# Optimization experiments

Measured on AMD Instinct MI355X. Metric: run time of the kernel, lower is better.

Reference implementation:

```python
import jax, jax.numpy as jnp
import numpy as np

N = 100000        # nodes
E = 1600000       # directed edges (before self loops)
F = 128           # input node features
H1, H2, H3 = 64, 32, 16
G = 64            # graphs in batch
EPS = 1e-5
NEG_SLOPE = 0.2


def setup_inputs():
    key = jax.random.key(0)
    ks = jax.random.split(key, 16)
    def rn(k, shape, scale=1.0):
        return jax.random.normal(k, shape, dtype=jnp.float32) * scale
    inp = {}
    inp['x'] = rn(ks[0], (N, F))
    inp['edge_index'] = jax.random.randint(ks[1], (2, E), 0, N)
    inp['batch'] = jnp.sort(jax.random.randint(ks[2], (N,), 0, G))
    dims = [(F, H1), (H1, H2), (H2, H3)]
    i = 3
    for li, (fi, fo) in enumerate(dims, start=1):
        s = 1.0 / np.sqrt(fi)
        kk = jax.random.split(ks[i], 3)
        inp[f'Wl{li}'] = rn(kk[0], (fi, fo), s)
        inp[f'bl{li}'] = jnp.zeros((fo,), jnp.float32)
        inp[f'Wr{li}'] = rn(kk[1], (fi, fo), s)
        inp[f'br{li}'] = jnp.zeros((fo,), jnp.float32)
        inp[f'att{li}'] = rn(kk[2], (fo,), 1.0 / np.sqrt(fo))
        inp[f'bias{li}'] = jnp.zeros((fo,), jnp.float32)
        inp[f'gamma{li}'] = jnp.ones((fo,), jnp.float32)
        inp[f'beta{li}'] = jnp.zeros((fo,), jnp.float32)
        i += 1
    inp['linW'] = rn(ks[i], (H3, 1), 0.25)
    inp['linb'] = jnp.zeros((1,), jnp.float32)
    return inp


def _gatv2(x, Wl, bl, Wr, br, att, bias, src, dst):
    # PyG GATv2Conv, heads=1: e_ij = a^T LeakyReLU(Wl x_j + Wr x_i)
    xl = x @ Wl + bl                         # [N, H] source transform
    xr = x @ Wr + br                         # [N, H] target transform
    e = jax.nn.leaky_relu(xl[src] + xr[dst], NEG_SLOPE) @ att   # [E']
    # numerically stable segment softmax over incoming edges of dst
    emax = jax.ops.segment_max(e, dst, num_segments=N)
    w = jnp.exp(e - emax[dst])
    denom = jax.ops.segment_sum(w, dst, num_segments=N)
    alpha = w / (denom[dst] + 1e-16)         # [E']
    out = jax.ops.segment_sum(alpha[:, None] * xl[src], dst, num_segments=N)
    return out + bias


def _batchnorm(x, gamma, beta):
    mu = jnp.mean(x, axis=0)
    var = jnp.var(x, axis=0)
    return (x - mu) * jax.lax.rsqrt(var + EPS) * gamma + beta


def reference(x, edge_index, batch,
              Wl1, bl1, Wr1, br1, att1, bias1, gamma1, beta1,
              Wl2, bl2, Wr2, br2, att2, bias2, gamma2, beta2,
              Wl3, bl3, Wr3, br3, att3, bias3, gamma3, beta3,
              linW, linb):
    # add self loops once (PyG GATv2Conv default add_self_loops=True)
    loops = jnp.arange(N, dtype=edge_index.dtype)
    src = jnp.concatenate([edge_index[0], loops])
    dst = jnp.concatenate([edge_index[1], loops])

    h = _gatv2(x, Wl1, bl1, Wr1, br1, att1, bias1, src, dst)
    h = jax.nn.relu(_batchnorm(h, gamma1, beta1))
    h = _gatv2(h, Wl2, bl2, Wr2, br2, att2, bias2, src, dst)
    h = jax.nn.relu(_batchnorm(h, gamma2, beta2))
    h = _gatv2(h, Wl3, bl3, Wr3, br3, att3, bias3, src, dst)
    h = jax.nn.relu(_batchnorm(h, gamma3, beta3))

    # global mean pool over graphs
    sums = jax.ops.segment_sum(h, batch, num_segments=G)          # [G, 16]
    cnts = jax.ops.segment_sum(jnp.ones((N,), h.dtype), batch, num_segments=G)
    pooled = sums / jnp.maximum(cnts, 1.0)[:, None]
    return pooled @ linW + linb                                   # [G, 1]
```

## Files before the change

kernel.cpp:

```cpp
#include <hip/hip_runtime.h>
#include <hip/hip_bf16.h>


static constexpr int G_ = 64;

typedef short bfrag __attribute__((ext_vector_type(8)));
typedef float facc  __attribute__((ext_vector_type(4)));

__device__ __forceinline__ float asfloat_(unsigned int u) {
  union { unsigned int i; float f; } c; c.i = u; return c.f;
}
__device__ __forceinline__ unsigned short f2bf(float f) {
  union { float f; unsigned int i; } c;
  c.f = f;
  unsigned int r = c.i + 0x7FFFu + ((c.i >> 16) & 1u);
  return (unsigned short)(r >> 16);
}

__device__ __forceinline__ void load_bf4(const unsigned short* p, float* f) {
  uint2 q = *reinterpret_cast<const uint2*>(p);
  f[0] = asfloat_(q.x << 16); f[1] = asfloat_(q.x & 0xFFFF0000u);
  f[2] = asfloat_(q.y << 16); f[3] = asfloat_(q.y & 0xFFFF0000u);
}

__global__ __launch_bounds__(256) void pack_all(
    const float* __restrict__ Wl1, const float* __restrict__ Wr1,
    const float* __restrict__ bl1, const float* __restrict__ br1,
    const float* __restrict__ Wl2, const float* __restrict__ Wr2,
    const float* __restrict__ bl2, const float* __restrict__ br2,
    const float* __restrict__ Wl3, const float* __restrict__ Wr3,
    const float* __restrict__ bl3, const float* __restrict__ br3,
    unsigned short* __restrict__ Wt1, float* __restrict__ bc1,
    unsigned short* __restrict__ Wt2, float* __restrict__ bc2,
    unsigned short* __restrict__ Wt3, float* __restrict__ bc3) {
  int i = blockIdx.x * 256 + threadIdx.x;
  if (i < 128 * 128) { int c = i >> 7, k = i & 127;
    Wt1[i] = f2bf((c < 64) ? Wl1[k * 64 + c] : Wr1[k * 64 + (c - 64)]); }
  if (i < 128) bc1[i] = (i < 64) ? bl1[i] : br1[i - 64];
  if (i < 64 * 64) { int c = i >> 6, k = i & 63;
    Wt2[i] = f2bf((c < 32) ? Wl2[k * 32 + c] : Wr2[k * 32 + (c - 32)]); }
  if (i < 64) bc2[i] = (i < 32) ? bl2[i] : br2[i - 32];
  if (i < 32 * 32) { int c = i >> 5, k = i & 31;
    Wt3[i] = f2bf((c < 16) ? Wl3[k * 16 + c] : Wr3[k * 16 + (c - 16)]); }
  if (i < 32) bc3[i] = (i < 16) ? bl3[i] : br3[i - 16];
}

__global__ __launch_bounds__(256) void edge_hist(
    const int* __restrict__ ei, int* __restrict__ deg, int E, int Etot, int N) {
  int p = blockIdx.x & 7;
  int q = blockIdx.x >> 3;
  int nbq = gridDim.x >> 3;
  float scale = 8.0f / (float)N;
  for (int i = q * 256 + threadIdx.x; i < Etot; i += nbq * 256) {
    int dst = (i < E) ? ei[E + i] : (i - E);
    int pp = min((int)((float)dst * scale), 7);
    if (pp == p) atomicAdd(&deg[dst], 1);
  }
}

__global__ __launch_bounds__(256) void scan1(
    const int* __restrict__ deg, int* __restrict__ part, int* __restrict__ bsums, int n) {
  __shared__ int ts[256];
  int t = threadIdx.x, b = blockIdx.x;
  int base = b * 1024 + t * 4;
  int d[4];
#pragma unroll
  for (int q = 0; q < 4; q++) d[q] = (base + q < n) ? deg[base + q] : 0;
  int s = d[0] + d[1] + d[2] + d[3];
  ts[t] = s;
  __syncthreads();
  for (int o = 1; o < 256; o <<= 1) {
    int v = (t >= o) ? ts[t - o] : 0;
    __syncthreads();
    ts[t] += v;
    __syncthreads();
  }
  int incl = ts[t];
  if (t == 255) bsums[b] = incl;
  int run = incl - s;
#pragma unroll
  for (int q = 0; q < 4; q++) {
    if (base + q < n) part[base + q] = run;
    run += d[q];
  }
}

__global__ void scan2(int* bsums, int nb) {
  __shared__ int s[256];
  int t = threadIdx.x;
  int v = (t < nb) ? bsums[t] : 0;
  s[t] = v;
  __syncthreads();
  for (int o = 1; o < 256; o <<= 1) {
    int u = (t >= o) ? s[t - o] : 0;
    __syncthreads();
    s[t] += u;
    __syncthreads();
  }
  if (t < nb) bsums[t] = s[t] - v;
}

__global__ __launch_bounds__(256) void scan3(
    int* __restrict__ rp, int* __restrict__ cur, const int* __restrict__ bsums,
    int n, int Etot) {
  int i = blockIdx.x * 256 + threadIdx.x;
  if (i < n) {
    int v = rp[i] + bsums[i >> 10];
    rp[i] = v; cur[i] = v;
  }
  if (i == 0) rp[n] = Etot;
}

__global__ __launch_bounds__(256) void scatter_edges(
    const int* __restrict__ ei, int* __restrict__ cur, int* __restrict__ ssrc,
    int E, int Etot, int N) {
  int p = blockIdx.x & 7;
  int q = blockIdx.x >> 3;
  int nbq = gridDim.x >> 3;
  float scale = 8.0f / (float)N;
  for (int i = q * 256 + threadIdx.x; i < Etot; i += nbq * 256) {
    int dst = (i < E) ? ei[E + i] : (i - E);
    int pp = min((int)((float)dst * scale), 7);
    if (pp != p) continue;
    int src = (i < E) ? ei[i] : (i - E);
    int pos = atomicAdd(&cur[dst], 1);
    ssrc[pos] = src;
  }
}

template <int FI, int FO, int AMODE>
__global__ __launch_bounds__(256) void gemm_mfma(
    const void* __restrict__ Ain, const float* __restrict__ ssb,
    const unsigned short* __restrict__ Wt, const float* __restrict__ bcat,
    unsigned short* __restrict__ XL, unsigned short* __restrict__ XR, int N) {
  constexpr int NT = FO / 16;
  constexpr int KS = FI / 32;
  constexpr int H = FO / 2;
  int tid = threadIdx.x;
  int w = tid >> 6;
  int lr = tid & 15;
  int lg = (tid & 63) >> 4;
  int n0 = blockIdx.x * 64;
  int arow = min(n0 + w * 16 + lr, N - 1);

  facc acc[NT];
#pragma unroll
  for (int t = 0; t < NT; t++)
#pragma unroll
    for (int e = 0; e < 4; e++) acc[t][e] = 0.f;

#pragma unroll
  for (int ks = 0; ks < KS; ks++) {
    int k0 = ks * 32 + lg * 8;
    bfrag a;
    if constexpr (AMODE == 0) {
      const unsigned short* Ab = (const unsigned short*)Ain;
      a = *reinterpret_cast<const bfrag*>(&Ab[(size_t)arow * FI + k0]);
    } else {
      const float* Af = (const float*)Ain;
      const float* p = &Af[(size_t)arow * FI + k0];
      float4 lo = *reinterpret_cast<const float4*>(p);
      float4 hi = *reinterpret_cast<const float4*>(p + 4);
      float f[8] = {lo.x, lo.y, lo.z, lo.w, hi.x, hi.y, hi.z, hi.w};
      if constexpr (AMODE == 2) {
        float4 sc0 = *reinterpret_cast<const float4*>(&ssb[k0]);
        float4 sc1 = *reinterpret_cast<const float4*>(&ssb[k0 + 4]);
        float4 sh0 = *reinterpret_cast<const float4*>(&ssb[FI + k0]);
        float4 sh1 = *reinterpret_cast<const float4*>(&ssb[FI + k0 + 4]);
        float sc[8] = {sc0.x, sc0.y, sc0.z, sc0.w, sc1.x, sc1.y, sc1.z, sc1.w};
        float sh[8] = {sh0.x, sh0.y, sh0.z, sh0.w, sh1.x, sh1.y, sh1.z, sh1.w};
#pragma unroll
        for (int e = 0; e < 8; e++) f[e] = fmaxf(fmaf(f[e], sc[e], sh[e]), 0.f);
      }
      union { bfrag v; unsigned short u[8]; } cv;
#pragma unroll
      for (int e = 0; e < 8; e++) cv.u[e] = f2bf(f[e]);
      a = cv.v;
    }
#pragma unroll
    for (int t = 0; t < NT; t++) {
      bfrag b = *reinterpret_cast<const bfrag*>(&Wt[(size_t)(t * 16 + lr) * FI + k0]);
      acc[t] = __builtin_amdgcn_mfma_f32_16x16x32_bf16(a, b, acc[t], 0, 0, 0);
    }
  }

#pragma unroll
  for (int t = 0; t < NT; t++) {
    int col = t * 16 + lr;
    float bias = bcat[col];
    unsigned short* dstbuf = (t < NT / 2) ? XL : XR;
    int cc = (t < NT / 2) ? col : (col - H);
#pragma unroll
    for (int r = 0; r < 4; r++) {
      int n = n0 + w * 16 + lg * 4 + r;
      if (n < N) dstbuf[(size_t)n * H + cc] = f2bf(acc[t][r] + bias);
    }
  }
}

__device__ __forceinline__ float lrelu02(float z) {
  return fmaxf(z, 0.2f * z);
}

template <int H>
__global__ __launch_bounds__(256) void gat_agg5(
    const unsigned short* __restrict__ XL, const unsigned short* __restrict__ XR,
    const float* __restrict__ att, const float* __restrict__ bias,
    const int* __restrict__ rp, const int* __restrict__ ssrc,
    float* __restrict__ out, int N) {
  constexpr int L = H / 4;
  constexpr int C = 64 / L;
  constexpr int CHUNK = 128;
  __shared__ float ts[4][CHUNK];
  int wv = threadIdx.x >> 6;
  int v = blockIdx.x * 4 + wv;
  if (v >= N) return;
  int lane = threadIdx.x & 63;
  int fl = lane % L;
  int sub = lane / L;

  float xr[4];
  load_bf4(&XR[(size_t)v * H + fl * 4], xr);
  const float4 a4 = *reinterpret_cast<const float4*>(&att[fl * 4]);
  int beg = rp[v], end = rp[v + 1];

  float m = -3.0e38f, d = 0.f, acc[4] = {0.f, 0.f, 0.f, 0.f};

  for (int c0 = beg; c0 < end; c0 += CHUNK) {
    int n = min(CHUNK, end - c0);

    float mc = -3.0e38f;
    for (int k = sub; k < n; k += C) {
      int u = ssrc[c0 + k];
      float xl[4];
      load_bf4(&XL[(size_t)u * H + fl * 4], xl);
      float t = a4.x * lrelu02(xl[0] + xr[0]);
      t = fmaf(a4.y, lrelu02(xl[1] + xr[1]), t);
      t = fmaf(a4.z, lrelu02(xl[2] + xr[2]), t);
      t = fmaf(a4.w, lrelu02(xl[3] + xr[3]), t);
#pragma unroll
      for (int o = L / 2; o >= 1; o >>= 1) t += __shfl_xor(t, o);
      mc = fmaxf(mc, t);
      if (fl == 0) ts[wv][k] = t;
    }
#pragma unroll
    for (int o = L; o < 64; o <<= 1) mc = fmaxf(mc, __shfl_xor(mc, o));

    float mn = fmaxf(m, mc);
    float sc = __expf(m - mn);
    d *= sc;
#pragma unroll
    for (int e = 0; e < 4; e++) acc[e] *= sc;
    m = mn;

    float dl = 0.f;
    for (int k = lane; k < n; k += 64) {
      float w = __expf(ts[wv][k] - m);
      ts[wv][k] = w;
      dl += w;
    }
#pragma unroll
    for (int o = 1; o < 64; o <<= 1) dl += __shfl_xor(dl, o);
    d += dl;

    for (int k = sub; k < n; k += C) {
      float wgt = ts[wv][k];
      int u = ssrc[c0 + k];
      float xl[4];
      load_bf4(&XL[(size_t)u * H + fl * 4], xl);
#pragma unroll
      for (int e = 0; e < 4; e++) acc[e] = fmaf(wgt, xl[e], acc[e]);
    }
  }

#pragma unroll
  for (int o = L; o < 64; o <<= 1) {
#pragma unroll
    for (int e = 0; e < 4; e++) acc[e] += __shfl_xor(acc[e], o);
  }

  if (lane < L) {
    float inv = 1.f / (d + 1e-16f);
    const float4 b4 = *reinterpret_cast<const float4*>(&bias[fl * 4]);
    float4 o4 = make_float4(fmaf(acc[0], inv, b4.x), fmaf(acc[1], inv, b4.y),
                            fmaf(acc[2], inv, b4.z), fmaf(acc[3], inv, b4.w));
    *reinterpret_cast<float4*>(&out[(size_t)v * H + fl * 4]) = o4;
  }
}

template <int H>
__global__ __launch_bounds__(256) void bn_stats(
    const float* __restrict__ X, float* __restrict__ stats, int N) {
  __shared__ float ls[256], ls2[256];
  int tid = threadIdx.x;
  int h = tid % H;
  constexpr int RPB = 256 / H;
  int r0 = blockIdx.x * RPB + tid / H;
  float s = 0.f, s2 = 0.f;
  for (int n = r0; n < N; n += gridDim.x * RPB) {
    float val = X[(size_t)n * H + h];
    s += val; s2 += val * val;
  }
  ls[tid] = s; ls2[tid] = s2;
  __syncthreads();
  if (tid < H) {
    for (int g = 1; g < RPB; g++) { s += ls[tid + g * H]; s2 += ls2[tid + g * H]; }
    atomicAdd(&stats[h], s);
    atomicAdd(&stats[H + h], s2);
  }
}

__global__ void bn_finalize(
    const float* __restrict__ stats, const float* __restrict__ gamma,
    const float* __restrict__ beta, float* __restrict__ ss, int H, int N) {
  int h = threadIdx.x;
  if (h < H) {
    float mean = stats[h] / (float)N;
    float var = stats[H + h] / (float)N - mean * mean;
    float istd = rsqrtf(var + 1e-5f);
    float sc = gamma[h] * istd;
    ss[h] = sc;
    ss[H + h] = beta[h] - mean * sc;
  }
}

__global__ __launch_bounds__(256) void pool_kernel(
    const float* __restrict__ X, const float* __restrict__ ss,
    const int* __restrict__ batch, float* __restrict__ pool,
    float* __restrict__ cnt, int N) {
  __shared__ float lp[G_ * 16];
  __shared__ float lc[G_];
  int tid = threadIdx.x;
  for (int j = tid; j < G_ * 16; j += 256) lp[j] = 0.f;
  if (tid < G_) lc[tid] = 0.f;
  __syncthreads();
  int tot = N * 16;
  for (int i = blockIdx.x * 256 + tid; i < tot; i += gridDim.x * 256) {
    int n = i >> 4, h = i & 15;
    int g = batch[n];
    float t = X[i] * ss[h] + ss[16 + h];
    t = (t > 0.f) ? t : 0.f;
    atomicAdd(&lp[g * 16 + h], t);
    if (h == 0) atomicAdd(&lc[g], 1.0f);
  }
  __syncthreads();
  for (int j = tid; j < G_ * 16; j += 256) atomicAdd(&pool[j], lp[j]);
  if (tid < G_) atomicAdd(&cnt[tid], lc[tid]);
}

__global__ void final_linear(
    const float* __restrict__ pool, const float* __restrict__ cnt,
    const float* __restrict__ linW, const float* __restrict__ linb,
    float* __restrict__ out) {
  int g = threadIdx.x;
  if (g < G_) {
    float c = fmaxf(cnt[g], 1.0f);
    float acc = 0.f;
    for (int h = 0; h < 16; h++) acc += (pool[g * 16 + h] / c) * linW[h];
    out[g] = acc + linb[0];
  }
}

extern "C" void kernel_launch(void* const* d_in, const int* in_sizes, int n_in,
                              void* d_out, int out_size, void* d_ws, size_t ws_size,
                              hipStream_t stream) {
  const float* x = (const float*)d_in[0];
  const int* ei = (const int*)d_in[1];
  const int* batch = (const int*)d_in[2];
  const int N = in_sizes[0] / 128;
  const int E = in_sizes[1] / 2;
  const int Etot = E + N;

  char* wsb = (char*)d_ws;
  size_t off = 0;
  auto alloc = [&](size_t bytes) -> void* {
    void* p = wsb + off;
    off += (bytes + 255) & ~(size_t)255;
    return p;
  };
  unsigned short* XLb = (unsigned short*)alloc((size_t)64 * N * 2);
  unsigned short* XRb = (unsigned short*)alloc((size_t)64 * N * 2);
  float* R2 = (float*)alloc((size_t)64 * N * 4);
  int* row_ptr = (int*)alloc((size_t)(N + 1) * 4);
  int* cursor = (int*)alloc((size_t)N * 4);
  int* bsums = (int*)alloc(4096);
  int* ssrc = (int*)alloc((size_t)Etot * 4);
  unsigned short* Wt1 = (unsigned short*)alloc(16384 * 2);
  float* bc1 = (float*)alloc(128 * 4);
  unsigned short* Wt2 = (unsigned short*)alloc(4096 * 2);
  float* bc2 = (float*)alloc(64 * 4);
  unsigned short* Wt3 = (unsigned short*)alloc(1024 * 2);
  float* bc3 = (float*)alloc(32 * 4);
  float* ss = (float*)alloc(256 * 4);
  size_t zelems = (size_t)N + 3 * 128 + G_ * 16 + G_;
  char* zb = (char*)alloc(zelems * 4);
  int* deg = (int*)zb;
  float* stats1 = (float*)(zb + (size_t)N * 4);
  float* stats2 = stats1 + 128;
  float* stats3 = stats2 + 128;
  float* pool = stats3 + 128;
  float* cnt = pool + G_ * 16;

  const float* Wl1 = (const float*)d_in[3];  const float* bl1 = (const float*)d_in[4];
  const float* Wr1 = (const float*)d_in[5];  const float* br1 = (const float*)d_in[6];
  const float* att1 = (const float*)d_in[7]; const float* bias1 = (const float*)d_in[8];
  const float* g1 = (const float*)d_in[9];   const float* b1 = (const float*)d_in[10];
  const float* Wl2 = (const float*)d_in[11]; const float* bl2 = (const float*)d_in[12];
  const float* Wr2 = (const float*)d_in[13]; const float* br2 = (const float*)d_in[14];
  const float* att2 = (const float*)d_in[15]; const float* bias2 = (const float*)d_in[16];
  const float* g2 = (const float*)d_in[17];  const float* b2 = (const float*)d_in[18];
  const float* Wl3 = (const float*)d_in[19]; const float* bl3 = (const float*)d_in[20];
  const float* Wr3 = (const float*)d_in[21]; const float* br3 = (const float*)d_in[22];
  const float* att3 = (const float*)d_in[23]; const float* bias3 = (const float*)d_in[24];
  const float* g3 = (const float*)d_in[25];  const float* b3 = (const float*)d_in[26];
  const float* linW = (const float*)d_in[27]; const float* linb = (const float*)d_in[28];
  float* out = (float*)d_out;

  int nb = (N + 1023) / 1024;
  int nnodeblk = (N + 3) / 4;
  int ngemm = (N + 63) / 64;

  pack_all<<<64, 256, 0, stream>>>(Wl1, Wr1, bl1, br1, Wl2, Wr2, bl2, br2,
                                   Wl3, Wr3, bl3, br3, Wt1, bc1, Wt2, bc2, Wt3, bc3);
  hipMemsetAsync(zb, 0, zelems * 4, stream);

  edge_hist<<<4096, 256, 0, stream>>>(ei, deg, E, Etot, N);
  scan1<<<nb, 256, 0, stream>>>(deg, row_ptr, bsums, N);
  scan2<<<1, 256, 0, stream>>>(bsums, nb);
  scan3<<<(N + 255) / 256, 256, 0, stream>>>(row_ptr, cursor, bsums, N, Etot);
  scatter_edges<<<4096, 256, 0, stream>>>(ei, cursor, ssrc, E, Etot, N);

  gemm_mfma<128, 128, 1><<<ngemm, 256, 0, stream>>>(x, nullptr, Wt1, bc1, XLb, XRb, N);
  gat_agg5<64><<<nnodeblk, 256, 0, stream>>>(XLb, XRb, att1, bias1, row_ptr, ssrc, R2, N);
  bn_stats<64><<<512, 256, 0, stream>>>(R2, stats1, N);
  bn_finalize<<<1, 64, 0, stream>>>(stats1, g1, b1, ss, 64, N);

  gemm_mfma<64, 64, 2><<<ngemm, 256, 0, stream>>>(R2, ss, Wt2, bc2, XLb, XRb, N);
  gat_agg5<32><<<nnodeblk, 256, 0, stream>>>(XLb, XRb, att2, bias2, row_ptr, ssrc, R2, N);
  bn_stats<32><<<512, 256, 0, stream>>>(R2, stats2, N);
  bn_finalize<<<1, 64, 0, stream>>>(stats2, g2, b2, ss, 32, N);

  gemm_mfma<32, 32, 2><<<ngemm, 256, 0, stream>>>(R2, ss, Wt3, bc3, XLb, XRb, N);
  gat_agg5<16><<<nnodeblk, 256, 0, stream>>>(XLb, XRb, att3, bias3, row_ptr, ssrc, R2, N);
  bn_stats<16><<<512, 256, 0, stream>>>(R2, stats3, N);
  bn_finalize<<<1, 64, 0, stream>>>(stats3, g3, b3, ss, 16, N);

  pool_kernel<<<2048, 256, 0, stream>>>(R2, ss, batch, pool, cnt, N);
  final_linear<<<1, 64, 0, stream>>>(pool, cnt, linW, linb, out);
}
```

Measured before the change: 578.3 us.

## Keep gathered neighbor features in registers and fuse softmax passes in GAT aggregation

The aggregation kernel now loads each chunk of neighbor features once into registers (ITER edges per lane group). It computes scores, the online max, the exp weights and the weighted accumulation from those registers. This drops the shared-memory score buffer and the second gather of XL per edge. The denominator is kept per lane group and reduced with shuffles at the end. The costs are more registers per thread and wasted lanes when a node's degree is not a multiple of the chunk size; per-layer ITER values are chosen to balance these.

After: 502.4 us. 13.1% less time.

```diff
diff --git a/kernel.cpp b/kernel.cpp
--- a/kernel.cpp
+++ b/kernel.cpp
@@ -202,18 +202,16 @@
   return fmaxf(z, 0.2f * z);
 }
 
-template <int H>
-__global__ __launch_bounds__(256) void gat_agg5(
+template <int H, int ITER>
+__global__ __launch_bounds__(256) void gat_agg6(
     const unsigned short* __restrict__ XL, const unsigned short* __restrict__ XR,
     const float* __restrict__ att, const float* __restrict__ bias,
     const int* __restrict__ rp, const int* __restrict__ ssrc,
     float* __restrict__ out, int N) {
   constexpr int L = H / 4;
   constexpr int C = 64 / L;
-  constexpr int CHUNK = 128;
-  __shared__ float ts[4][CHUNK];
-  int wv = threadIdx.x >> 6;
-  int v = blockIdx.x * 4 + wv;
+  constexpr int CHUNK = C * ITER;
+  int v = blockIdx.x * 4 + (threadIdx.x >> 6);
   if (v >= N) return;
   int lane = threadIdx.x & 63;
   int fl = lane % L;
@@ -226,22 +224,25 @@
 
   float m = -3.0e38f, d = 0.f, acc[4] = {0.f, 0.f, 0.f, 0.f};
 
-  for (int c0 = beg; c0 < end; c0 += CHUNK) {
-    int n = min(CHUNK, end - c0);
-
+  for (int cb = beg; cb < end; cb += CHUNK) {
+    float xb[ITER][4];
+    float tl[ITER];
     float mc = -3.0e38f;
-    for (int k = sub; k < n; k += C) {
-      int u = ssrc[c0 + k];
-      float xl[4];
-      load_bf4(&XL[(size_t)u * H + fl * 4], xl);
-      float t = a4.x * lrelu02(xl[0] + xr[0]);
-      t = fmaf(a4.y, lrelu02(xl[1] + xr[1]), t);
-      t = fmaf(a4.z, lrelu02(xl[2] + xr[2]), t);
-      t = fmaf(a4.w, lrelu02(xl[3] + xr[3]), t);
+#pragma unroll
+    for (int it = 0; it < ITER; it++) {
+      int j = cb + it * C + sub;
+      bool valid = (j < end);
+      int jj = valid ? j : (end - 1);
+      int u = ssrc[jj];
+      load_bf4(&XL[(size_t)u * H + fl * 4], xb[it]);
+      float t = a4.x * lrelu02(xb[it][0] + xr[0]);
+      t = fmaf(a4.y, lrelu02(xb[it][1] + xr[1]), t);
+      t = fmaf(a4.z, lrelu02(xb[it][2] + xr[2]), t);
+      t = fmaf(a4.w, lrelu02(xb[it][3] + xr[3]), t);
 #pragma unroll
       for (int o = L / 2; o >= 1; o >>= 1) t += __shfl_xor(t, o);
-      mc = fmaxf(mc, t);
-      if (fl == 0) ts[wv][k] = t;
+      tl[it] = valid ? t : -3.0e38f;
+      mc = fmaxf(mc, tl[it]);
     }
 #pragma unroll
     for (int o = L; o < 64; o <<= 1) mc = fmaxf(mc, __shfl_xor(mc, o));
@@ -253,28 +254,18 @@
     for (int e = 0; e < 4; e++) acc[e] *= sc;
     m = mn;
 
-    float dl = 0.f;
-    for (int k = lane; k < n; k += 64) {
-      float w = __expf(ts[wv][k] - m);
-      ts[wv][k] = w;
-      dl += w;
+#pragma unroll
+    for (int it = 0; it < ITER; it++) {
+      float w = __expf(tl[it] - m);
+      d += w;
+#pragma unroll
+      for (int e = 0; e < 4; e++) acc[e] = fmaf(w, xb[it][e], acc[e]);
     }
-#pragma unroll
-    for (int o = 1; o < 64; o <<= 1) dl += __shfl_xor(dl, o);
-    d += dl;
-
-    for (int k = sub; k < n; k += C) {
-      float wgt = ts[wv][k];
-      int u = ssrc[c0 + k];
-      float xl[4];
-      load_bf4(&XL[(size_t)u * H + fl * 4], xl);
-#pragma unroll
-      for (int e = 0; e < 4; e++) acc[e] = fmaf(wgt, xl[e], acc[e]);
-    }
   }
 
 #pragma unroll
   for (int o = L; o < 64; o <<= 1) {
+    d += __shfl_xor(d, o);
 #pragma unroll
     for (int e = 0; e < 4; e++) acc[e] += __shfl_xor(acc[e], o);
   }
@@ -431,17 +422,17 @@
   scatter_edges<<<4096, 256, 0, stream>>>(ei, cursor, ssrc, E, Etot, N);
 
   gemm_mfma<128, 128, 1><<<ngemm, 256, 0, stream>>>(x, nullptr, Wt1, bc1, XLb, XRb, N);
-  gat_agg5<64><<<nnodeblk, 256, 0, stream>>>(XLb, XRb, att1, bias1, row_ptr, ssrc, R2, N);
+  gat_agg6<64, 6><<<nnodeblk, 256, 0, stream>>>(XLb, XRb, att1, bias1, row_ptr, ssrc, R2, N);
   bn_stats<64><<<512, 256, 0, stream>>>(R2, stats1, N);
   bn_finalize<<<1, 64, 0, stream>>>(stats1, g1, b1, ss, 64, N);
 
   gemm_mfma<64, 64, 2><<<ngemm, 256, 0, stream>>>(R2, ss, Wt2, bc2, XLb, XRb, N);
-  gat_agg5<32><<<nnodeblk, 256, 0, stream>>>(XLb, XRb, att2, bias2, row_ptr, ssrc, R2, N);
+  gat_agg6<32, 4><<<nnodeblk, 256, 0, stream>>>(XLb, XRb, att2, bias2, row_ptr, ssrc, R2, N);
   bn_stats<32><<<512, 256, 0, stream>>>(R2, stats2, N);
   bn_finalize<<<1, 64, 0, stream>>>(stats2, g2, b2, ss, 32, N);
 
   gemm_mfma<32, 32, 2><<<ngemm, 256, 0, stream>>>(R2, ss, Wt3, bc3, XLb, XRb, N);
-  gat_agg5<16><<<nnodeblk, 256, 0, stream>>>(XLb, XRb, att3, bias3, row_ptr, ssrc, R2, N);
+  gat_agg6<16, 2><<<nnodeblk, 256, 0, stream>>>(XLb, XRb, att3, bias3, row_ptr, ssrc, R2, N);
   bn_stats<16><<<512, 256, 0, stream>>>(R2, stats3, N);
   bn_finalize<<<1, 64, 0, stream>>>(stats3, g3, b3, ss, 16, N);
 
```
